# Optimization experiments

Measured on AMD Instinct MI355X. Metric: run time of the kernel, lower is better.

## Reference

```python
import jax, jax.numpy as jnp
import numpy as np

IN_CH = 512
OUT_CH = 512
KSIZE = 7
PAD = 3
EPS = 1e-6
QP = 127.0
QN = -128.0


def setup_inputs() -> dict:
    key = jax.random.key(0)
    k1, k2, k3 = jax.random.split(key, 3)
    x = jax.random.normal(k1, (8, IN_CH, 8192), dtype=jnp.float32)
    # kaiming_uniform_(a=sqrt(5)) ~ U(-bound, bound), bound = sqrt(6/((1+5)*fan_in)) = 1/sqrt(fan_in)
    fan_in = IN_CH * KSIZE
    bound = 1.0 / np.sqrt(fan_in)
    weight = jax.random.uniform(k2, (OUT_CH, IN_CH, KSIZE), dtype=jnp.float32,
                                minval=-bound, maxval=bound)
    norm_weight = jnp.ones((IN_CH,), dtype=jnp.float32)
    return {"x": x, "weight": weight, "norm_weight": norm_weight}


def _rmsnorm(x_bct, gamma):
    # RMSNorm over channel dim; module transposes to (B, T, C) and normalizes last axis.
    xt = jnp.swapaxes(x_bct, 1, 2)  # (B, T, C)
    rms = jax.lax.rsqrt(jnp.mean(xt * xt, axis=-1, keepdims=True) + EPS)
    xt = xt * rms * gamma
    return jnp.swapaxes(xt, 1, 2)  # (B, C, T)


def _act_quant_8bit(x):
    x = jnp.nan_to_num(x, nan=0.0, posinf=1e4, neginf=-1e4)
    scale = jnp.maximum(jnp.max(jnp.abs(x)), 1e-5)
    x_scaled = x / scale * QP
    x_quant = jnp.round(jnp.clip(x_scaled, QN, QP))
    x_quant = jax.lax.stop_gradient(x_quant - x_scaled) + x_scaled  # STE
    return x_quant / QP * scale


def _weight_quant_ternary(w):
    scale = jnp.maximum(jnp.mean(jnp.abs(w)), 1e-4)
    w_norm = w / scale
    w_q = jnp.round(jnp.clip(w_norm, -1.0, 1.0))
    w_q = jax.lax.stop_gradient(w_q - w_norm) + w_norm  # STE
    return w_q, scale


def reference(x, weight, norm_weight):
    x = _rmsnorm(x, norm_weight)
    x_q = _act_quant_8bit(x)
    w_q, w_scale = _weight_quant_ternary(weight)
    out = jax.lax.conv_general_dilated(
        x_q, w_q,
        window_strides=(1,),
        padding=[(PAD, PAD)],
        lhs_dilation=(1,),
        rhs_dilation=(1,),
        dimension_numbers=("NCH", "OIH", "NCH"),
    )
    return out * w_scale
```

## Files before the change

kernel.cpp:

```cpp
#include <hip/hip_runtime.h>
#include <stdint.h>

#define B_ 8
#define C_ 512
#define O_ 512
#define T_ 8192
#define KW 7
#define NW (O_*C_*KW)
#define QT_ROWS (T_+32)
#define MT 64
#define NT 256
#define BK 64
#define BROWS 272
#define WSUM_BLKS 1792
#define RMS_BLKS (B_ * (T_/64))

typedef __attribute__((ext_vector_type(4))) int i32x4;

__device__ __forceinline__ void gld16(const void* g, void* l) {
  __builtin_amdgcn_global_load_lds(
      (const __attribute__((address_space(1))) unsigned int*)g,
      (__attribute__((address_space(3))) unsigned int*)l, 16, 0, 0);
}

__global__ __launch_bounds__(256) void k_rms(const float* __restrict__ x,
    const float* __restrict__ gamma, float* __restrict__ rms,
    unsigned* __restrict__ smax)
{
  int tid = threadIdx.x, tl = tid & 63, cg = tid >> 6;
  int tt0 = blockIdx.x * 64;
  int b   = blockIdx.y;
  int t   = tt0 + tl;
  const float* px = x + ((size_t)b * C_ + cg * 128) * T_ + t;
  const float* pg = gamma + cg * 128;
  float ss = 0.f, mx = 0.f;
  #pragma unroll 8
  for (int cc = 0; cc < 128; ++cc) {
    float v = px[(size_t)cc * T_];
    float g = pg[cc];
    ss = fmaf(v, v, ss);
    mx = fmaxf(mx, fabsf(v * g));
  }
  __shared__ float s_ss[4][64];
  __shared__ float s_m[4][64];
  s_ss[cg][tl] = ss; s_m[cg][tl] = mx;
  __syncthreads();
  if (cg == 0) {
    float r = 1.0f / sqrtf(
        (s_ss[0][tl] + s_ss[1][tl] + s_ss[2][tl] + s_ss[3][tl]) *
        (1.0f / 512.0f) + 1e-6f);
    rms[(size_t)b * T_ + t] = r;
    float mm = fmaxf(fmaxf(s_m[0][tl], s_m[1][tl]),
                     fmaxf(s_m[2][tl], s_m[3][tl])) * r;
    #pragma unroll
    for (int off = 32; off > 0; off >>= 1)
      mm = fmaxf(mm, __shfl_down(mm, off));
    if (tl == 0)
      smax[blockIdx.y * (T_/64) + blockIdx.x] = __float_as_uint(mm);
  }
}

__global__ __launch_bounds__(256) void k_wsum(const float* __restrict__ w,
    float* __restrict__ wpart, char* __restrict__ qa)
{
  int tid = threadIdx.x;
  if (blockIdx.x < 32) {
    int g4 = blockIdx.x * 256 + tid;
    int b = g4 >> 10;
    int idx = (g4 & 1023) * 4;
    int rr = idx >> 9, c = idx & 511;
    int row = (rr < 4) ? rr : (T_ + rr);
    *(unsigned*)&qa[((size_t)b * QT_ROWS + row) * C_ + c] = 0u;
  }
  size_t g = (size_t)blockIdx.x * 256 + tid;
  float s = 0.f;
  for (size_t i = g; i < (size_t)NW; i += (size_t)gridDim.x * 256)
    s += fabsf(w[i]);
  __shared__ float red[256];
  red[tid] = s; __syncthreads();
  for (int h = 128; h > 0; h >>= 1) {
    if (tid < h) red[tid] += red[tid + h];
    __syncthreads();
  }
  if (tid == 0) wpart[blockIdx.x] = red[0];
}

__global__ __launch_bounds__(256) void k_red(const float* __restrict__ wpart,
    const unsigned* __restrict__ smax, double* __restrict__ wsum,
    unsigned* __restrict__ scale_bits)
{
  int tid = threadIdx.x;
  double s = 0.0;
  for (int i = tid; i < WSUM_BLKS; i += 256) s += (double)wpart[i];
  unsigned m = 0u;
  for (int i = tid; i < RMS_BLKS; i += 256) m = max(m, smax[i]);
  __shared__ double sd[256];
  __shared__ unsigned su[256];
  sd[tid] = s; su[tid] = m; __syncthreads();
  for (int h = 128; h > 0; h >>= 1) {
    if (tid < h) { sd[tid] += sd[tid + h]; su[tid] = max(su[tid], su[tid + h]); }
    __syncthreads();
  }
  if (tid == 0) { *wsum = sd[0]; *scale_bits = su[0]; }
}

__global__ __launch_bounds__(256) void k_wq(const float* __restrict__ w,
    const double* __restrict__ wsum, char* __restrict__ wqi)
{
  int g = blockIdx.x * 256 + threadIdx.x;
  float wsc = fmaxf((float)(*wsum * (1.0 / (double)NW)), 1e-4f);
  const float* pw = w + (size_t)g * KW;
  #pragma unroll
  for (int kk = 0; kk < KW; ++kk) {
    float q = rintf(fminf(fmaxf(pw[kk] / wsc, -1.f), 1.f));
    wqi[(size_t)kk * (O_ * C_) + g] = (char)(int)q;
  }
}

__global__ __launch_bounds__(256) void k_quant(const float* __restrict__ x,
    const float* __restrict__ gamma, const float* __restrict__ rms,
    const unsigned* __restrict__ scale_bits, char* __restrict__ qa)
{
  __shared__ float tile[64][65];
  int tid = threadIdx.x;
  int tt0 = blockIdx.x * 64;
  int c0  = blockIdx.y * 64;
  int b   = blockIdx.z;
  float qmul = 127.0f / fmaxf(__uint_as_float(*scale_bits), 1e-5f);
  int t4 = (tid & 15) * 4;
  const float* px = x + ((size_t)b * C_ + c0) * T_ + tt0;
  float4 rr = *(const float4*)(rms + (size_t)b * T_ + tt0 + t4);
  #pragma unroll
  for (int p = 0; p < 4; ++p) {
    int cc = (tid >> 4) + p * 16;
    float4 v = *(const float4*)(px + (size_t)cc * T_ + t4);
    float g = gamma[c0 + cc];
    tile[cc][t4 + 0] = rintf(fminf(fmaxf(((v.x * rr.x) * g) * qmul, -128.f), 127.f));
    tile[cc][t4 + 1] = rintf(fminf(fmaxf(((v.y * rr.y) * g) * qmul, -128.f), 127.f));
    tile[cc][t4 + 2] = rintf(fminf(fmaxf(((v.z * rr.z) * g) * qmul, -128.f), 127.f));
    tile[cc][t4 + 3] = rintf(fminf(fmaxf(((v.w * rr.w) * g) * qmul, -128.f), 127.f));
  }
  __syncthreads();
  int c16 = (tid & 3) * 16, t2 = tid >> 2;
  unsigned u[4];
  #pragma unroll
  for (int d = 0; d < 4; ++d)
    u[d] = ((unsigned)(unsigned char)(char)(int)tile[c16 + d * 4 + 0][t2])
         | ((unsigned)(unsigned char)(char)(int)tile[c16 + d * 4 + 1][t2] << 8)
         | ((unsigned)(unsigned char)(char)(int)tile[c16 + d * 4 + 2][t2] << 16)
         | ((unsigned)(unsigned char)(char)(int)tile[c16 + d * 4 + 3][t2] << 24);
  char* pq = qa + ((size_t)b * QT_ROWS + (tt0 + 4 + t2)) * C_ + c0 + c16;
  *(uint4*)pq = make_uint4(u[0], u[1], u[2], u[3]);
}

__global__ __launch_bounds__(256, 3) void k_conv(
    const char* __restrict__ wqi,
    const char* __restrict__ qa,
    float* __restrict__ out,
    const unsigned* __restrict__ scale_bits,
    const double* __restrict__ wsum)
{
  __shared__ __attribute__((aligned(16))) char lA[KW * 64 * BK];
  __shared__ __attribute__((aligned(16))) char lB[BROWS * BK];
  int tid = threadIdx.x;
  int wave = tid >> 6, lane = tid & 63;
  int quad = lane >> 4, l16 = lane & 15;
  int lrow = lane >> 2;
  int dch = ((lane & 3) - (lane >> 3)) & 3;
  int t0 = blockIdx.x * NT;
  int o0 = blockIdx.y * MT;
  int b  = blockIdx.z;

  const char* qa_b = qa + (size_t)b * QT_ROWS * C_;

  i32x4 acc[4][4] = {};

  for (int c0 = 0; c0 < C_; c0 += BK) {
    for (int i = wave; i < 17; i += 4) {
      const char* gB = qa_b + (size_t)(t0 + i * 16 + lrow) * C_ + (c0 + dch * 16);
      gld16(gB, &lB[i * 1024 + lane * 16]);
    }
    for (int i = wave; i < 28; i += 4) {
      int k = i >> 2, ii = i & 3;
      const char* gA =
          wqi + (size_t)(k * O_ + o0 + ii * 16 + lrow) * C_ + (c0 + dch * 16);
      gld16(gA, &lA[i * 1024 + lane * 16]);
    }
    __syncthreads();
    #pragma unroll
    for (int k = 0; k < KW; ++k) {
      i32x4 af[4], bf[4];
      #pragma unroll
      for (int mt = 0; mt < 4; ++mt) {
        int r = mt * 16 + l16;
        af[mt] = *(const i32x4*)
            &lA[k * 4096 + r * BK + (((quad + (r >> 1)) & 3) * 16)];
      }
      int sft = k + 1;
      #pragma unroll
      for (int nt = 0; nt < 4; ++nt) {
        int r = wave * 64 + nt * 16 + l16 + sft;
        bf[nt] = *(const i32x4*)
            &lB[r * BK + (((quad + (r >> 1)) & 3) * 16)];
      }
      __builtin_amdgcn_s_setprio(1);
      #pragma unroll
      for (int mt = 0; mt < 4; ++mt)
        #pragma unroll
        for (int nt = 0; nt < 4; ++nt)
          acc[mt][nt] = __builtin_amdgcn_mfma_i32_16x16x64_i8(
              af[mt], bf[nt], acc[mt][nt], 0, 0, 0);
      __builtin_amdgcn_s_setprio(0);
    }
    __syncthreads();
  }
  float sc  = fmaxf(__uint_as_float(*scale_bits), 1e-5f);
  float wsc = fmaxf((float)(*wsum * (1.0 / (double)NW)), 1e-4f);
  float alpha = sc * (1.0f / 127.0f) * wsc;
  #pragma unroll
  for (int mt = 0; mt < 4; ++mt) {
    int o = o0 + mt * 16 + quad * 4;
    #pragma unroll
    for (int nt = 0; nt < 4; ++nt) {
      int t = t0 + wave * 64 + nt * 16 + l16;
      float* po = out + ((size_t)b * O_ + o) * T_ + t;
      #pragma unroll
      for (int r2 = 0; r2 < 4; ++r2)
        po[(size_t)r2 * T_] = (float)acc[mt][nt][r2] * alpha;
    }
  }
}

extern "C" void kernel_launch(void* const* d_in, const int* in_sizes, int n_in,
                              void* d_out, int out_size, void* d_ws, size_t ws_size,
                              hipStream_t stream)
{
  const float* x     = (const float*)d_in[0];
  const float* w     = (const float*)d_in[1];
  const float* gamma = (const float*)d_in[2];
  float* out = (float*)d_out;
  char* ws = (char*)d_ws;
  unsigned* scale_bits = (unsigned*)ws;
  double*   wsum       = (double*)(ws + 16);
  float*    rms        = (float*)(ws + 256);
  char*     wqi        = (char*)(ws + 262400);
  float*    wpart      = (float*)(ws + 262400);
  unsigned* smax       = (unsigned*)(ws + 262400 + 8192);
  char*     qa         = (char*)(ws + 2359552);

  k_rms  <<<dim3(T_/64, B_),        256, 0, stream>>>(x, gamma, rms, smax);
  k_wsum <<<dim3(WSUM_BLKS),        256, 0, stream>>>(w, wpart, qa);
  k_red  <<<dim3(1),                256, 0, stream>>>(wpart, smax, wsum, scale_bits);
  k_wq   <<<dim3(O_*C_/256),        256, 0, stream>>>(w, wsum, wqi);
  k_quant<<<dim3(T_/64, C_/64, B_), 256, 0, stream>>>(x, gamma, rms, scale_bits, qa);
  k_conv <<<dim3(T_/NT, O_/MT, B_), 256, 0, stream>>>(wqi, qa, out, scale_bits, wsum);
}
```

Before: 350.0 us.

## Switch conv to 32x32x32 int8 MFMA and merge preprocessing kernels

The conv inner loop moves from 16x16x64 int8 MFMA tiles to 32x32x32 int8 MFMA, with 2x2 accumulators of 16 ints each per wave. The fragment loads and the output index mapping are rewritten for the 32-row layout. Separately, the rms and weight-sum kernels are merged into one launch, and the weight-quant and activation-quant kernels into another, cutting launches from six to four. The larger MFMA shape aims for better issue efficiency, but the output stores become less coalesced per register and the LDS access pattern changes.

```diff
diff --git a/kernel.cpp b/kernel.cpp
--- a/kernel.cpp
+++ b/kernel.cpp
@@ -15,7 +15,8 @@
 #define WSUM_BLKS 1792
 #define RMS_BLKS (B_ * (T_/64))
 
-typedef __attribute__((ext_vector_type(4))) int i32x4;
+typedef __attribute__((ext_vector_type(4)))  int i32x4;
+typedef __attribute__((ext_vector_type(16))) int i32x16;
 
 __device__ __forceinline__ void gld16(const void* g, void* l) {
   __builtin_amdgcn_global_load_lds(
@@ -23,66 +24,64 @@
       (__attribute__((address_space(3))) unsigned int*)l, 16, 0, 0);
 }
 
-__global__ __launch_bounds__(256) void k_rms(const float* __restrict__ x,
-    const float* __restrict__ gamma, float* __restrict__ rms,
-    unsigned* __restrict__ smax)
-{
-  int tid = threadIdx.x, tl = tid & 63, cg = tid >> 6;
-  int tt0 = blockIdx.x * 64;
-  int b   = blockIdx.y;
-  int t   = tt0 + tl;
-  const float* px = x + ((size_t)b * C_ + cg * 128) * T_ + t;
-  const float* pg = gamma + cg * 128;
-  float ss = 0.f, mx = 0.f;
-  #pragma unroll 8
-  for (int cc = 0; cc < 128; ++cc) {
-    float v = px[(size_t)cc * T_];
-    float g = pg[cc];
-    ss = fmaf(v, v, ss);
-    mx = fmaxf(mx, fabsf(v * g));
-  }
-  __shared__ float s_ss[4][64];
-  __shared__ float s_m[4][64];
-  s_ss[cg][tl] = ss; s_m[cg][tl] = mx;
-  __syncthreads();
-  if (cg == 0) {
-    float r = 1.0f / sqrtf(
-        (s_ss[0][tl] + s_ss[1][tl] + s_ss[2][tl] + s_ss[3][tl]) *
-        (1.0f / 512.0f) + 1e-6f);
-    rms[(size_t)b * T_ + t] = r;
-    float mm = fmaxf(fmaxf(s_m[0][tl], s_m[1][tl]),
-                     fmaxf(s_m[2][tl], s_m[3][tl])) * r;
-    #pragma unroll
-    for (int off = 32; off > 0; off >>= 1)
-      mm = fmaxf(mm, __shfl_down(mm, off));
-    if (tl == 0)
-      smax[blockIdx.y * (T_/64) + blockIdx.x] = __float_as_uint(mm);
-  }
-}
-
-__global__ __launch_bounds__(256) void k_wsum(const float* __restrict__ w,
+__global__ __launch_bounds__(256) void k_rmsw(const float* __restrict__ x,
+    const float* __restrict__ gamma, const float* __restrict__ w,
+    float* __restrict__ rms, unsigned* __restrict__ smax,
     float* __restrict__ wpart, char* __restrict__ qa)
 {
-  int tid = threadIdx.x;
-  if (blockIdx.x < 32) {
-    int g4 = blockIdx.x * 256 + tid;
-    int b = g4 >> 10;
-    int idx = (g4 & 1023) * 4;
-    int rr = idx >> 9, c = idx & 511;
-    int row = (rr < 4) ? rr : (T_ + rr);
-    *(unsigned*)&qa[((size_t)b * QT_ROWS + row) * C_ + c] = 0u;
-  }
-  size_t g = (size_t)blockIdx.x * 256 + tid;
-  float s = 0.f;
-  for (size_t i = g; i < (size_t)NW; i += (size_t)gridDim.x * 256)
-    s += fabsf(w[i]);
-  __shared__ float red[256];
-  red[tid] = s; __syncthreads();
-  for (int h = 128; h > 0; h >>= 1) {
-    if (tid < h) red[tid] += red[tid + h];
-    __syncthreads();
-  }
-  if (tid == 0) wpart[blockIdx.x] = red[0];
+  int bx = blockIdx.x, tid = threadIdx.x;
+  if (bx < RMS_BLKS) {
+    int tl = tid & 63, cg = tid >> 6;
+    int b = bx >> 7, tt0 = (bx & 127) * 64;
+    int t = tt0 + tl;
+    const float* px = x + ((size_t)b * C_ + cg * 128) * T_ + t;
+    const float* pg = gamma + cg * 128;
+    float ss = 0.f, mx = 0.f;
+    #pragma unroll 8
+    for (int cc = 0; cc < 128; ++cc) {
+      float v = px[(size_t)cc * T_];
+      float g = pg[cc];
+      ss = fmaf(v, v, ss);
+      mx = fmaxf(mx, fabsf(v * g));
+    }
+    __shared__ float s_ss[4][64];
+    __shared__ float s_m[4][64];
+    s_ss[cg][tl] = ss; s_m[cg][tl] = mx;
+    __syncthreads();
+    if (cg == 0) {
+      float r = 1.0f / sqrtf(
+          (s_ss[0][tl] + s_ss[1][tl] + s_ss[2][tl] + s_ss[3][tl]) *
+          (1.0f / 512.0f) + 1e-6f);
+      rms[(size_t)b * T_ + t] = r;
+      float mm = fmaxf(fmaxf(s_m[0][tl], s_m[1][tl]),
+                       fmaxf(s_m[2][tl], s_m[3][tl])) * r;
+      #pragma unroll
+      for (int off = 32; off > 0; off >>= 1)
+        mm = fmaxf(mm, __shfl_down(mm, off));
+      if (tl == 0) smax[bx] = __float_as_uint(mm);
+    }
+  } else {
+    int wb = bx - RMS_BLKS;
+    if (wb < 32) {
+      int g4 = wb * 256 + tid;
+      int b = g4 >> 10;
+      int idx = (g4 & 1023) * 4;
+      int rr = idx >> 9, c = idx & 511;
+      int row = (rr < 4) ? rr : (T_ + rr);
+      *(unsigned*)&qa[((size_t)b * QT_ROWS + row) * C_ + c] = 0u;
+    }
+    size_t g = (size_t)wb * 256 + tid;
+    float s = 0.f;
+    for (size_t i = g; i < (size_t)NW; i += (size_t)WSUM_BLKS * 256)
+      s += fabsf(w[i]);
+    __shared__ float red[256];
+    red[tid] = s; __syncthreads();
+    for (int h = 128; h > 0; h >>= 1) {
+      if (tid < h) red[tid] += red[tid + h];
+      __syncthreads();
+    }
+    if (tid == 0) wpart[wb] = red[0];
+  }
 }
 
 __global__ __launch_bounds__(256) void k_red(const float* __restrict__ wpart,
@@ -104,28 +103,29 @@
   if (tid == 0) { *wsum = sd[0]; *scale_bits = su[0]; }
 }
 
-__global__ __launch_bounds__(256) void k_wq(const float* __restrict__ w,
-    const double* __restrict__ wsum, char* __restrict__ wqi)
-{
-  int g = blockIdx.x * 256 + threadIdx.x;
-  float wsc = fmaxf((float)(*wsum * (1.0 / (double)NW)), 1e-4f);
-  const float* pw = w + (size_t)g * KW;
-  #pragma unroll
-  for (int kk = 0; kk < KW; ++kk) {
-    float q = rintf(fminf(fmaxf(pw[kk] / wsc, -1.f), 1.f));
-    wqi[(size_t)kk * (O_ * C_) + g] = (char)(int)q;
-  }
-}
-
-__global__ __launch_bounds__(256) void k_quant(const float* __restrict__ x,
-    const float* __restrict__ gamma, const float* __restrict__ rms,
-    const unsigned* __restrict__ scale_bits, char* __restrict__ qa)
+__global__ __launch_bounds__(256) void k_wqq(const float* __restrict__ w,
+    const double* __restrict__ wsum, char* __restrict__ wqi,
+    const float* __restrict__ x, const float* __restrict__ gamma,
+    const float* __restrict__ rms, const unsigned* __restrict__ scale_bits,
+    char* __restrict__ qa)
 {
   __shared__ float tile[64][65];
-  int tid = threadIdx.x;
-  int tt0 = blockIdx.x * 64;
-  int c0  = blockIdx.y * 64;
-  int b   = blockIdx.z;
+  int bx = blockIdx.x, tid = threadIdx.x;
+  if (bx < 1024) {
+    int g = bx * 256 + tid;
+    float wsc = fmaxf((float)(*wsum * (1.0 / (double)NW)), 1e-4f);
+    const float* pw = w + (size_t)g * KW;
+    #pragma unroll
+    for (int kk = 0; kk < KW; ++kk) {
+      float q = rintf(fminf(fmaxf(pw[kk] / wsc, -1.f), 1.f));
+      wqi[(size_t)kk * (O_ * C_) + g] = (char)(int)q;
+    }
+    return;
+  }
+  int qx = bx - 1024;
+  int tt0 = (qx & 127) * 64;
+  int c0  = ((qx >> 7) & 7) * 64;
+  int b   = qx >> 10;
   float qmul = 127.0f / fmaxf(__uint_as_float(*scale_bits), 1e-5f);
   int t4 = (tid & 15) * 4;
   const float* px = x + ((size_t)b * C_ + c0) * T_ + tt0;
@@ -164,7 +164,7 @@
   __shared__ __attribute__((aligned(16))) char lB[BROWS * BK];
   int tid = threadIdx.x;
   int wave = tid >> 6, lane = tid & 63;
-  int quad = lane >> 4, l16 = lane & 15;
+  int l31 = lane & 31, khg = lane >> 5;
   int lrow = lane >> 2;
   int dch = ((lane & 3) - (lane >> 3)) & 3;
   int t0 = blockIdx.x * NT;
@@ -173,7 +173,7 @@
 
   const char* qa_b = qa + (size_t)b * QT_ROWS * C_;
 
-  i32x4 acc[4][4] = {};
+  i32x16 acc[2][2] = {};
 
   for (int c0 = 0; c0 < C_; c0 += BK) {
     for (int i = wave; i < 17; i += 4) {
@@ -189,27 +189,37 @@
     __syncthreads();
     #pragma unroll
     for (int k = 0; k < KW; ++k) {
-      i32x4 af[4], bf[4];
-      #pragma unroll
-      for (int mt = 0; mt < 4; ++mt) {
-        int r = mt * 16 + l16;
-        af[mt] = *(const i32x4*)
-            &lA[k * 4096 + r * BK + (((quad + (r >> 1)) & 3) * 16)];
-      }
+      i32x4 af[2][2], bf[2][2];
+      #pragma unroll
+      for (int mt = 0; mt < 2; ++mt)
+        #pragma unroll
+        for (int kh = 0; kh < 2; ++kh) {
+          int r = mt * 32 + l31;
+          int g = kh * 2 + khg;
+          af[mt][kh] = *(const i32x4*)
+              &lA[k * 4096 + r * BK + (((g + (r >> 1)) & 3) * 16)];
+        }
       int sft = k + 1;
       #pragma unroll
-      for (int nt = 0; nt < 4; ++nt) {
-        int r = wave * 64 + nt * 16 + l16 + sft;
-        bf[nt] = *(const i32x4*)
-            &lB[r * BK + (((quad + (r >> 1)) & 3) * 16)];
+      for (int nt = 0; nt < 2; ++nt) {
+        #pragma unroll
+        for (int kh = 0; kh < 2; ++kh) {
+          int r = wave * 64 + nt * 32 + l31 + sft;
+          int g = kh * 2 + khg;
+          bf[nt][kh] = *(const i32x4*)
+              &lB[r * BK + (((g + (r >> 1)) & 3) * 16)];
+        }
       }
       __builtin_amdgcn_s_setprio(1);
       #pragma unroll
-      for (int mt = 0; mt < 4; ++mt)
+      for (int mt = 0; mt < 2; ++mt)
         #pragma unroll
-        for (int nt = 0; nt < 4; ++nt)
-          acc[mt][nt] = __builtin_amdgcn_mfma_i32_16x16x64_i8(
-              af[mt], bf[nt], acc[mt][nt], 0, 0, 0);
+        for (int nt = 0; nt < 2; ++nt) {
+          acc[mt][nt] = __builtin_amdgcn_mfma_i32_32x32x32_i8(
+              af[mt][0], bf[nt][0], acc[mt][nt], 0, 0, 0);
+          acc[mt][nt] = __builtin_amdgcn_mfma_i32_32x32x32_i8(
+              af[mt][1], bf[nt][1], acc[mt][nt], 0, 0, 0);
+        }
       __builtin_amdgcn_s_setprio(0);
     }
     __syncthreads();
@@ -218,15 +228,15 @@
   float wsc = fmaxf((float)(*wsum * (1.0 / (double)NW)), 1e-4f);
   float alpha = sc * (1.0f / 127.0f) * wsc;
   #pragma unroll
-  for (int mt = 0; mt < 4; ++mt) {
-    int o = o0 + mt * 16 + quad * 4;
+  for (int mt = 0; mt < 2; ++mt) {
     #pragma unroll
-    for (int nt = 0; nt < 4; ++nt) {
-      int t = t0 + wave * 64 + nt * 16 + l16;
-      float* po = out + ((size_t)b * O_ + o) * T_ + t;
-      #pragma unroll
-      for (int r2 = 0; r2 < 4; ++r2)
-        po[(size_t)r2 * T_] = (float)acc[mt][nt][r2] * alpha;
+    for (int nt = 0; nt < 2; ++nt) {
+      int t = t0 + wave * 64 + nt * 32 + l31;
+      #pragma unroll
+      for (int rg = 0; rg < 16; ++rg) {
+        int o = o0 + mt * 32 + (rg & 3) + 8 * (rg >> 2) + 4 * khg;
+        out[((size_t)b * O_ + o) * T_ + t] = (float)acc[mt][nt][rg] * alpha;
+      }
     }
   }
 }
@@ -248,10 +258,8 @@
   unsigned* smax       = (unsigned*)(ws + 262400 + 8192);
   char*     qa         = (char*)(ws + 2359552);
 
-  k_rms  <<<dim3(T_/64, B_),        256, 0, stream>>>(x, gamma, rms, smax);
-  k_wsum <<<dim3(WSUM_BLKS),        256, 0, stream>>>(w, wpart, qa);
-  k_red  <<<dim3(1),                256, 0, stream>>>(wpart, smax, wsum, scale_bits);
-  k_wq   <<<dim3(O_*C_/256),        256, 0, stream>>>(w, wsum, wqi);
-  k_quant<<<dim3(T_/64, C_/64, B_), 256, 0, stream>>>(x, gamma, rms, scale_bits, qa);
-  k_conv <<<dim3(T_/NT, O_/MT, B_), 256, 0, stream>>>(wqi, qa, out, scale_bits, wsum);
-}
+  k_rmsw <<<dim3(RMS_BLKS + WSUM_BLKS), 256, 0, stream>>>(x, gamma, w, rms, smax, wpart, qa);
+  k_red  <<<dim3(1),                    256, 0, stream>>>(wpart, smax, wsum, scale_bits);
+  k_wqq  <<<dim3(1024 + T_/64*8*B_),    256, 0, stream>>>(w, wsum, wqi, x, gamma, rms, scale_bits, qa);
+  k_conv <<<dim3(T_/NT, O_/MT, B_),     256, 0, stream>>>(wqi, qa, out, scale_bits, wsum);
+}
```

Result: slower. 369.4 us (+5.5%).
